# Kernel tuning notes

Measured on AMD Instinct MI355X. Metric: run time of the kernel, lower is better.

## Reference

```python
import jax, jax.numpy as jnp
import numpy as np

SIGMA = 0.1  # kernel-point influence radius (KPConv linear correlation)


def setup_inputs() -> dict:
    key = jax.random.key(0)
    k1, k2, k3, k4, k5 = jax.random.split(key, 5)
    N, K, KP, CIN, COUT = 65536, 32, 15, 64, 128
    pos = jax.random.uniform(k1, (N, 3), dtype=jnp.float32)
    feats = jax.random.normal(k2, (N, CIN), dtype=jnp.float32)
    kernel_points = jax.random.normal(k3, (KP, 3), dtype=jnp.float32) * 0.05
    weights = jax.random.normal(k4, (KP, CIN, COUT), dtype=jnp.float32) / np.sqrt(KP * CIN)
    neighbors = jax.random.randint(k5, (N, K), 0, N, dtype=jnp.int64)
    return {"pos": pos, "feats": feats, "kernel_points": kernel_points,
            "weights": weights, "neighbors": neighbors}


def reference(pos, feats, kernel_points, weights, neighbors):
    # pos: [N,3], feats: [N,Cin], kernel_points: [Kp,3],
    # weights: [Kp,Cin,Cout], neighbors: [N,K] int
    neigh_pos = pos[neighbors]                      # [N,K,3] irregular gather
    rel = neigh_pos - pos[:, None, :]               # [N,K,3]
    # distance from each relative neighbor offset to each kernel point
    d = rel[:, :, None, :] - kernel_points[None, None, :, :]   # [N,K,Kp,3]
    dist = jnp.sqrt(jnp.sum(d * d, axis=-1))        # [N,K,Kp]
    infl = jnp.maximum(0.0, 1.0 - dist / SIGMA)     # linear correlation
    neigh_feat = feats[neighbors]                   # [N,K,Cin] irregular gather
    # per-kernel-point weighted neighbor aggregation, then projection
    weighted = jnp.einsum('njk,njc->nkc', infl, neigh_feat)    # [N,Kp,Cin]
    out = jnp.einsum('nkc,kcd->nd', weighted, weights)         # [N,Cout]
    return out
```

## Files before the change

### kernel.cpp

```cpp
#include <hip/hip_runtime.h>

#define NPTS  65536
#define KNB   32
#define KPn   15
#define CIN   64
#define COUT  128
#define MPTS  16
#define THREADS 256
#define WSTRIDE 968
#define BCAP  32
#define NTILE 8
#define KSTEPS 30

typedef __attribute__((ext_vector_type(8))) short short8;
typedef __attribute__((ext_vector_type(4))) float f32x4;

__device__ __forceinline__ unsigned int f2bf(float f) {
    union { float f; unsigned int i; } v; v.f = f;
    return (v.i + 0x7fffu + ((v.i >> 16) & 1u)) >> 16;
}

__global__ void wtrans_kernel(const float* __restrict__ w,
                              unsigned short* __restrict__ wTf) {
    const int d = blockIdx.x * 256 + threadIdx.x;
    if (d < NTILE * KSTEPS * 64 * 8) {
        const int j    = d & 7;
        const int lane = (d >> 3) & 63;
        const int ks   = (d >> 9) % KSTEPS;
        const int t    = d / (KSTEPS * 512);
        const int f    = ks * 32 + (lane >> 4) * 8 + j;
        const int cg   = f / 120;
        const int rem  = f - cg * 120;
        const int kpk  = rem >> 3;
        const int cw   = rem & 7;
        const int orig = kpk * 64 + cg * 8 + cw;
        const int n    = t * 16 + (lane & 15);
        wTf[d] = (unsigned short)f2bf(w[(size_t)orig * COUT + n]);
    }
}

__global__ __launch_bounds__(THREADS, 4) void kpconv_kernel(
    const float* __restrict__ pos,
    const float* __restrict__ feats,
    const float* __restrict__ kpts,
    const unsigned short* __restrict__ wTf,
    const int*   __restrict__ neighbors,
    float*       __restrict__ out)
{
    __shared__ unsigned short wl[MPTS * WSTRIDE];
    __shared__ int   bcnt[MPTS];
    __shared__ int   bid[MPTS][BCAP];
    __shared__ float bval[MPTS][BCAP];
    __shared__ float cposf[MPTS * 3];
    __shared__ float kpfl[KPn * 3];

    const int tid = threadIdx.x;
    const int n0  = blockIdx.x * MPTS;

    if (tid < MPTS) bcnt[tid] = 0;
    if (tid < MPTS * 3) cposf[tid] = pos[(size_t)n0 * 3 + tid];
    if (tid < KPn * 3)  kpfl[tid]  = kpts[tid];
    __syncthreads();

    for (int s = tid; s < MPTS * KNB; s += THREADS) {
        const int p  = s >> 5;
        const int nb = neighbors[(size_t)n0 * KNB + s];
        const float rx = pos[(size_t)nb * 3 + 0] - cposf[p * 3 + 0];
        const float ry = pos[(size_t)nb * 3 + 1] - cposf[p * 3 + 1];
        const float rz = pos[(size_t)nb * 3 + 2] - cposf[p * 3 + 2];
        #pragma unroll
        for (int k = 0; k < KPn; ++k) {
            const float dx = rx - kpfl[k * 3 + 0];
            const float dy = ry - kpfl[k * 3 + 1];
            const float dz = rz - kpfl[k * 3 + 2];
            const float d2 = dx * dx + dy * dy + dz * dz;
            if (d2 < 0.01f) {
                const float w = 1.0f - 10.0f * sqrtf(d2);
                const int idx = atomicAdd(&bcnt[p], 1);
                if (idx < BCAP) { bid[p][idx] = (nb << 4) | k; bval[p][idx] = w; }
            }
        }
    }
    __syncthreads();

    #pragma unroll
    for (int it = 0; it < 8; ++it) {
        const int wi = tid + it * THREADS;
        const int cg = wi & 7;
        const int k  = (wi >> 3) & 15;
        const int p  = wi >> 7;
        if (k < KPn) {
            float a0=0.f,a1=0.f,a2=0.f,a3=0.f,a4=0.f,a5=0.f,a6=0.f,a7=0.f;
            const int cnt = min(bcnt[p], BCAP);
            for (int e = 0; e < cnt; ++e) {
                const int id = bid[p][e];
                if ((id & 15) == k) {
                    const float wv = bval[p][e];
                    const float* fr = feats + (size_t)(id >> 4) * CIN + cg * 8;
                    const float4 f0 = *(const float4*)fr;
                    const float4 f1 = *(const float4*)(fr + 4);
                    a0 += wv * f0.x; a1 += wv * f0.y; a2 += wv * f0.z; a3 += wv * f0.w;
                    a4 += wv * f1.x; a5 += wv * f1.y; a6 += wv * f1.z; a7 += wv * f1.w;
                }
            }
            uint4 u;
            u.x = f2bf(a0) | (f2bf(a1) << 16);
            u.y = f2bf(a2) | (f2bf(a3) << 16);
            u.z = f2bf(a4) | (f2bf(a5) << 16);
            u.w = f2bf(a6) | (f2bf(a7) << 16);
            *(uint4*)(wl + p * WSTRIDE + cg * 120 + k * 8) = u;
        }
    }
    __syncthreads();

    {
        const int wave = tid >> 6;
        const int lane = tid & 63;
        const int m    = lane & 15;
        const int q    = lane >> 4;

        f32x4 acc0 = {0.f, 0.f, 0.f, 0.f};
        f32x4 acc1 = {0.f, 0.f, 0.f, 0.f};

        const unsigned short* ap = wl + m * WSTRIDE + q * 8;
        const short8* bp0 = (const short8*)wTf + (size_t)(2 * wave) * KSTEPS * 64 + lane;
        const short8* bp1 = bp0 + (size_t)KSTEPS * 64;

        #pragma unroll 3
        for (int ks = 0; ks < KSTEPS; ++ks, ap += 32) {
            const short8 a  = *(const short8*)ap;
            const short8 b0 = bp0[ks * 64];
            const short8 b1 = bp1[ks * 64];
            acc0 = __builtin_amdgcn_mfma_f32_16x16x32_bf16(a, b0, acc0, 0, 0, 0);
            acc1 = __builtin_amdgcn_mfma_f32_16x16x32_bf16(a, b1, acc1, 0, 0, 0);
        }

        const int nb0 = wave * 32;
        #pragma unroll
        for (int r = 0; r < 4; ++r) {
            const size_t row = (size_t)(n0 + q * 4 + r) * COUT;
            out[row + nb0 + m]      = acc0[r];
            out[row + nb0 + 16 + m] = acc1[r];
        }
    }
}

extern "C" void kernel_launch(void* const* d_in, const int* in_sizes, int n_in,
                              void* d_out, int out_size, void* d_ws, size_t ws_size,
                              hipStream_t stream) {
    const float* pos       = (const float*)d_in[0];
    const float* feats     = (const float*)d_in[1];
    const float* kpts      = (const float*)d_in[2];
    const float* weights   = (const float*)d_in[3];
    const int*   neighbors = (const int*)d_in[4];
    float*       out       = (float*)d_out;
    unsigned short* wTf    = (unsigned short*)d_ws;

    wtrans_kernel<<<(NTILE * KSTEPS * 512 + 255) / 256, 256, 0, stream>>>(weights, wTf);
    kpconv_kernel<<<NPTS / MPTS, THREADS, 0, stream>>>(pos, feats, kpts, wTf, neighbors, out);
}
```

Measured before the change: 151.5 us.

## Double points per block, add bounding-sphere cull and dot-product kernel-point test

Doubles the block to 32 points and 512 threads. Each of the 8 waves now computes one 16-column output tile for two 16-row point tiles, so every weight B-fragment loaded from global memory is reused twice. The neighbor/kernel-point distance test first culls neighbors outside a bounding sphere (sigma plus the max kernel-point radius). It then uses a precomputed |kp|^2 and a dot-product comparison instead of computing full distances, which skips most of the 15-point loop. Shared memory per block roughly doubles (about 62 KB), which may lower occupancy. Launch bounds of 512x4 may not be achievable.

```diff
diff --git a/kernel.cpp b/kernel.cpp
--- a/kernel.cpp
+++ b/kernel.cpp
@@ -5,8 +5,8 @@
 #define KPn   15
 #define CIN   64
 #define COUT  128
-#define MPTS  16
-#define THREADS 256
+#define MPTS  32
+#define THREADS 512
 #define WSTRIDE 968
 #define BCAP  32
 #define NTILE 8
@@ -52,32 +52,57 @@
     __shared__ int   bid[MPTS][BCAP];
     __shared__ float bval[MPTS][BCAP];
     __shared__ float cposf[MPTS * 3];
-    __shared__ float kpfl[KPn * 3];
+    __shared__ float4 kpq[KPn];
+    __shared__ float R2s;
 
     const int tid = threadIdx.x;
     const int n0  = blockIdx.x * MPTS;
 
     if (tid < MPTS) bcnt[tid] = 0;
     if (tid < MPTS * 3) cposf[tid] = pos[(size_t)n0 * 3 + tid];
-    if (tid < KPn * 3)  kpfl[tid]  = kpts[tid];
+    if (tid < KPn) {
+        const float x = kpts[tid * 3 + 0];
+        const float y = kpts[tid * 3 + 1];
+        const float z = kpts[tid * 3 + 2];
+        kpq[tid] = make_float4(x, y, z, x * x + y * y + z * z);
+    }
+    if (tid == THREADS - 1) {
+        float mx = 0.f;
+        for (int k = 0; k < KPn; ++k) {
+            const float x = kpts[k * 3 + 0];
+            const float y = kpts[k * 3 + 1];
+            const float z = kpts[k * 3 + 2];
+            mx = fmaxf(mx, x * x + y * y + z * z);
+        }
+        const float R = 0.1f + sqrtf(mx);
+        R2s = R * R;
+    }
     __syncthreads();
 
-    for (int s = tid; s < MPTS * KNB; s += THREADS) {
-        const int p  = s >> 5;
-        const int nb = neighbors[(size_t)n0 * KNB + s];
-        const float rx = pos[(size_t)nb * 3 + 0] - cposf[p * 3 + 0];
-        const float ry = pos[(size_t)nb * 3 + 1] - cposf[p * 3 + 1];
-        const float rz = pos[(size_t)nb * 3 + 2] - cposf[p * 3 + 2];
+    {
+        const float R2 = R2s;
         #pragma unroll
-        for (int k = 0; k < KPn; ++k) {
-            const float dx = rx - kpfl[k * 3 + 0];
-            const float dy = ry - kpfl[k * 3 + 1];
-            const float dz = rz - kpfl[k * 3 + 2];
-            const float d2 = dx * dx + dy * dy + dz * dz;
-            if (d2 < 0.01f) {
-                const float w = 1.0f - 10.0f * sqrtf(d2);
-                const int idx = atomicAdd(&bcnt[p], 1);
-                if (idx < BCAP) { bid[p][idx] = (nb << 4) | k; bval[p][idx] = w; }
+        for (int it = 0; it < MPTS * KNB / THREADS; ++it) {
+            const int s  = tid + it * THREADS;
+            const int p  = s >> 5;
+            const int nb = neighbors[(size_t)n0 * KNB + s];
+            const float rx = pos[(size_t)nb * 3 + 0] - cposf[p * 3 + 0];
+            const float ry = pos[(size_t)nb * 3 + 1] - cposf[p * 3 + 1];
+            const float rz = pos[(size_t)nb * 3 + 2] - cposf[p * 3 + 2];
+            const float d2r = rx * rx + ry * ry + rz * rz;
+            if (d2r < R2) {
+                const float hd = 0.5f * (d2r - 0.01f);
+                #pragma unroll
+                for (int k = 0; k < KPn; ++k) {
+                    const float4 kp = kpq[k];
+                    const float dot = rx * kp.x + ry * kp.y + rz * kp.z;
+                    if (dot > hd + 0.5f * kp.w) {
+                        const float d2 = fmaxf(d2r - 2.f * dot + kp.w, 0.f);
+                        const float w = 1.0f - 10.0f * sqrtf(d2);
+                        const int idx = atomicAdd(&bcnt[p], 1);
+                        if (idx < BCAP) { bid[p][idx] = (nb << 4) | k; bval[p][idx] = w; }
+                    }
+                }
             }
         }
     }
@@ -122,25 +147,24 @@
         f32x4 acc0 = {0.f, 0.f, 0.f, 0.f};
         f32x4 acc1 = {0.f, 0.f, 0.f, 0.f};
 
-        const unsigned short* ap = wl + m * WSTRIDE + q * 8;
-        const short8* bp0 = (const short8*)wTf + (size_t)(2 * wave) * KSTEPS * 64 + lane;
-        const short8* bp1 = bp0 + (size_t)KSTEPS * 64;
+        const unsigned short* a0p = wl + m * WSTRIDE + q * 8;
+        const unsigned short* a1p = a0p + 16 * WSTRIDE;
+        const short8* bp = (const short8*)wTf + (size_t)wave * KSTEPS * 64 + lane;
 
         #pragma unroll 3
-        for (int ks = 0; ks < KSTEPS; ++ks, ap += 32) {
-            const short8 a  = *(const short8*)ap;
-            const short8 b0 = bp0[ks * 64];
-            const short8 b1 = bp1[ks * 64];
-            acc0 = __builtin_amdgcn_mfma_f32_16x16x32_bf16(a, b0, acc0, 0, 0, 0);
-            acc1 = __builtin_amdgcn_mfma_f32_16x16x32_bf16(a, b1, acc1, 0, 0, 0);
+        for (int ks = 0; ks < KSTEPS; ++ks, a0p += 32, a1p += 32) {
+            const short8 a0 = *(const short8*)a0p;
+            const short8 a1 = *(const short8*)a1p;
+            const short8 b  = bp[ks * 64];
+            acc0 = __builtin_amdgcn_mfma_f32_16x16x32_bf16(a0, b, acc0, 0, 0, 0);
+            acc1 = __builtin_amdgcn_mfma_f32_16x16x32_bf16(a1, b, acc1, 0, 0, 0);
         }
 
-        const int nb0 = wave * 32;
+        const int c = wave * 16 + m;
         #pragma unroll
         for (int r = 0; r < 4; ++r) {
-            const size_t row = (size_t)(n0 + q * 4 + r) * COUT;
-            out[row + nb0 + m]      = acc0[r];
-            out[row + nb0 + 16 + m] = acc1[r];
+            out[(size_t)(n0 + q * 4 + r) * COUT + c]      = acc0[r];
+            out[(size_t)(n0 + 16 + q * 4 + r) * COUT + c] = acc1[r];
         }
     }
 }
```

New measurement: 155.5 us. 2.7% more time.

## Fuse weight transform into a persistent KPConv kernel with a grid barrier

Applied to the files above, without the earlier changes.

Folds the bf16 weight re-layout into the main kernel and drops the separate launch. All blocks synchronise through a global atomic counter that waits on a poisoned-workspace sentinel. The grid becomes 512 persistent blocks of 512 threads, each looping over 8 point tiles, with each wave computing one 16-column output tile. Neighbor bucket entries are packed into one 32-bit word holding the neighbor index, the kernel-point index and a 12-bit quantized influence, which halves bucket LDS traffic. In exchange it depends on all blocks being co-resident, on the workspace counter state across calls, and on N being at most 65536, and it adds quantization error to the influence weights.

```diff
diff --git a/kernel.cpp b/kernel.cpp
--- a/kernel.cpp
+++ b/kernel.cpp
@@ -6,11 +6,15 @@
 #define CIN   64
 #define COUT  128
 #define MPTS  16
-#define THREADS 256
+#define THREADS 512
+#define GRID  512
+#define TPB   8
 #define WSTRIDE 968
-#define BCAP  32
+#define BCAP  48
 #define NTILE 8
 #define KSTEPS 30
+#define WELEMS (NTILE * KSTEPS * 64 * 8)
+#define POISON 0xAAAAAAAAu
 
 typedef __attribute__((ext_vector_type(8))) short short8;
 typedef __attribute__((ext_vector_type(4))) float f32x4;
@@ -20,128 +24,143 @@
     return (v.i + 0x7fffu + ((v.i >> 16) & 1u)) >> 16;
 }
 
-__global__ void wtrans_kernel(const float* __restrict__ w,
-                              unsigned short* __restrict__ wTf) {
-    const int d = blockIdx.x * 256 + threadIdx.x;
-    if (d < NTILE * KSTEPS * 64 * 8) {
-        const int j    = d & 7;
-        const int lane = (d >> 3) & 63;
-        const int ks   = (d >> 9) % KSTEPS;
-        const int t    = d / (KSTEPS * 512);
-        const int f    = ks * 32 + (lane >> 4) * 8 + j;
-        const int cg   = f / 120;
-        const int rem  = f - cg * 120;
-        const int kpk  = rem >> 3;
-        const int cw   = rem & 7;
-        const int orig = kpk * 64 + cg * 8 + cw;
-        const int n    = t * 16 + (lane & 15);
-        wTf[d] = (unsigned short)f2bf(w[(size_t)orig * COUT + n]);
-    }
-}
-
-__global__ __launch_bounds__(THREADS, 4) void kpconv_kernel(
+__global__ __launch_bounds__(THREADS, 2) void kpconv_kernel(
     const float* __restrict__ pos,
     const float* __restrict__ feats,
     const float* __restrict__ kpts,
-    const unsigned short* __restrict__ wTf,
+    const float* __restrict__ weights,
     const int*   __restrict__ neighbors,
-    float*       __restrict__ out)
+    float*       __restrict__ out,
+    unsigned short* __restrict__ wTf,
+    unsigned int* cnt)
 {
     __shared__ unsigned short wl[MPTS * WSTRIDE];
+    __shared__ unsigned int  bpk[MPTS][BCAP];
     __shared__ int   bcnt[MPTS];
-    __shared__ int   bid[MPTS][BCAP];
-    __shared__ float bval[MPTS][BCAP];
     __shared__ float cposf[MPTS * 3];
     __shared__ float kpfl[KPn * 3];
 
     const int tid = threadIdx.x;
-    const int n0  = blockIdx.x * MPTS;
 
-    if (tid < MPTS) bcnt[tid] = 0;
-    if (tid < MPTS * 3) cposf[tid] = pos[(size_t)n0 * 3 + tid];
-    if (tid < KPn * 3)  kpfl[tid]  = kpts[tid];
+    {
+        const int d = blockIdx.x * THREADS + tid;
+        if (d < WELEMS) {
+            const int j    = d & 7;
+            const int lane = (d >> 3) & 63;
+            const int ks   = (d >> 9) % KSTEPS;
+            const int t    = d / (KSTEPS * 512);
+            const int f    = ks * 32 + (lane >> 4) * 8 + j;
+            const int cg   = f / 120;
+            const int rem  = f - cg * 120;
+            const int orig = (rem >> 3) * 64 + cg * 8 + (rem & 7);
+            const int n    = t * 16 + (lane & 15);
+            wTf[d] = (unsigned short)f2bf(weights[(size_t)orig * COUT + n]);
+        }
+    }
+
     __syncthreads();
-
-    for (int s = tid; s < MPTS * KNB; s += THREADS) {
-        const int p  = s >> 5;
-        const int nb = neighbors[(size_t)n0 * KNB + s];
-        const float rx = pos[(size_t)nb * 3 + 0] - cposf[p * 3 + 0];
-        const float ry = pos[(size_t)nb * 3 + 1] - cposf[p * 3 + 1];
-        const float rz = pos[(size_t)nb * 3 + 2] - cposf[p * 3 + 2];
-        #pragma unroll
-        for (int k = 0; k < KPn; ++k) {
-            const float dx = rx - kpfl[k * 3 + 0];
-            const float dy = ry - kpfl[k * 3 + 1];
-            const float dz = rz - kpfl[k * 3 + 2];
-            const float d2 = dx * dx + dy * dy + dz * dz;
-            if (d2 < 0.01f) {
-                const float w = 1.0f - 10.0f * sqrtf(d2);
-                const int idx = atomicAdd(&bcnt[p], 1);
-                if (idx < BCAP) { bid[p][idx] = (nb << 4) | k; bval[p][idx] = w; }
-            }
-        }
+    if (tid == 0) {
+        __builtin_amdgcn_fence(__ATOMIC_RELEASE, "agent");
+        unsigned int v = __hip_atomic_load(cnt, __ATOMIC_RELAXED,
+                                           __HIP_MEMORY_SCOPE_AGENT);
+        if (v == POISON) atomicCAS(cnt, POISON, 0u);
+        atomicAdd(cnt, 1u);
+        unsigned int x;
+        do {
+            __builtin_amdgcn_s_sleep(2);
+            x = __hip_atomic_load(cnt, __ATOMIC_RELAXED,
+                                  __HIP_MEMORY_SCOPE_AGENT);
+        } while (x == POISON || x < GRID);
+        __builtin_amdgcn_fence(__ATOMIC_ACQUIRE, "agent");
     }
     __syncthreads();
 
-    #pragma unroll
-    for (int it = 0; it < 8; ++it) {
-        const int wi = tid + it * THREADS;
-        const int cg = wi & 7;
-        const int k  = (wi >> 3) & 15;
-        const int p  = wi >> 7;
-        if (k < KPn) {
-            float a0=0.f,a1=0.f,a2=0.f,a3=0.f,a4=0.f,a5=0.f,a6=0.f,a7=0.f;
-            const int cnt = min(bcnt[p], BCAP);
-            for (int e = 0; e < cnt; ++e) {
-                const int id = bid[p][e];
-                if ((id & 15) == k) {
-                    const float wv = bval[p][e];
-                    const float* fr = feats + (size_t)(id >> 4) * CIN + cg * 8;
-                    const float4 f0 = *(const float4*)fr;
-                    const float4 f1 = *(const float4*)(fr + 4);
-                    a0 += wv * f0.x; a1 += wv * f0.y; a2 += wv * f0.z; a3 += wv * f0.w;
-                    a4 += wv * f1.x; a5 += wv * f1.y; a6 += wv * f1.z; a7 += wv * f1.w;
+    if (tid < KPn * 3) kpfl[tid] = kpts[tid];
+
+    for (int it8 = 0; it8 < TPB; ++it8) {
+        const int n0 = (blockIdx.x * TPB + it8) * MPTS;
+
+        if (tid < MPTS) bcnt[tid] = 0;
+        if (tid < MPTS * 3) cposf[tid] = pos[(size_t)n0 * 3 + tid];
+        __syncthreads();
+
+        {
+            const int s  = tid;
+            const int p  = s >> 5;
+            const int nb = neighbors[(size_t)n0 * KNB + s];
+            const float rx = pos[(size_t)nb * 3 + 0] - cposf[p * 3 + 0];
+            const float ry = pos[(size_t)nb * 3 + 1] - cposf[p * 3 + 1];
+            const float rz = pos[(size_t)nb * 3 + 2] - cposf[p * 3 + 2];
+            #pragma unroll
+            for (int k = 0; k < KPn; ++k) {
+                const float dx = rx - kpfl[k * 3 + 0];
+                const float dy = ry - kpfl[k * 3 + 1];
+                const float dz = rz - kpfl[k * 3 + 2];
+                const float d2 = dx * dx + dy * dy + dz * dz;
+                if (d2 < 0.01f) {
+                    const float w = 1.0f - 10.0f * sqrtf(d2);
+                    const unsigned int wq = (unsigned int)(w * 4095.0f + 0.5f);
+                    const int idx = atomicAdd(&bcnt[p], 1);
+                    if (idx < BCAP)
+                        bpk[p][idx] = ((unsigned int)nb << 16) | ((unsigned int)k << 12) | wq;
                 }
             }
-            uint4 u;
-            u.x = f2bf(a0) | (f2bf(a1) << 16);
-            u.y = f2bf(a2) | (f2bf(a3) << 16);
-            u.z = f2bf(a4) | (f2bf(a5) << 16);
-            u.w = f2bf(a6) | (f2bf(a7) << 16);
-            *(uint4*)(wl + p * WSTRIDE + cg * 120 + k * 8) = u;
         }
-    }
-    __syncthreads();
+        __syncthreads();
 
-    {
-        const int wave = tid >> 6;
-        const int lane = tid & 63;
-        const int m    = lane & 15;
-        const int q    = lane >> 4;
+        #pragma unroll
+        for (int it = 0; it < 4; ++it) {
+            const int wi = tid + it * THREADS;
+            const int cg = wi & 7;
+            const int k  = (wi >> 3) & 15;
+            const int p  = wi >> 7;
+            if (k < KPn) {
+                float a0=0.f,a1=0.f,a2=0.f,a3=0.f,a4=0.f,a5=0.f,a6=0.f,a7=0.f;
+                const int cnt2 = min(bcnt[p], BCAP);
+                for (int e = 0; e < cnt2; ++e) {
+                    const unsigned int id = bpk[p][e];
+                    if (((id >> 12) & 15u) == (unsigned int)k) {
+                        const float wv = (float)(id & 4095u) * (1.0f / 4095.0f);
+                        const float* fr = feats + (size_t)(id >> 16) * CIN + cg * 8;
+                        const float4 f0 = *(const float4*)fr;
+                        const float4 f1 = *(const float4*)(fr + 4);
+                        a0 += wv * f0.x; a1 += wv * f0.y; a2 += wv * f0.z; a3 += wv * f0.w;
+                        a4 += wv * f1.x; a5 += wv * f1.y; a6 += wv * f1.z; a7 += wv * f1.w;
+                    }
+                }
+                uint4 u;
+                u.x = f2bf(a0) | (f2bf(a1) << 16);
+                u.y = f2bf(a2) | (f2bf(a3) << 16);
+                u.z = f2bf(a4) | (f2bf(a5) << 16);
+                u.w = f2bf(a6) | (f2bf(a7) << 16);
+                *(uint4*)(wl + p * WSTRIDE + cg * 120 + k * 8) = u;
+            }
+        }
+        __syncthreads();
 
-        f32x4 acc0 = {0.f, 0.f, 0.f, 0.f};
-        f32x4 acc1 = {0.f, 0.f, 0.f, 0.f};
+        {
+            const int wave = tid >> 6;
+            const int lane = tid & 63;
+            const int m    = lane & 15;
+            const int q    = lane >> 4;
 
-        const unsigned short* ap = wl + m * WSTRIDE + q * 8;
-        const short8* bp0 = (const short8*)wTf + (size_t)(2 * wave) * KSTEPS * 64 + lane;
-        const short8* bp1 = bp0 + (size_t)KSTEPS * 64;
+            f32x4 acc = {0.f, 0.f, 0.f, 0.f};
+            const unsigned short* ap = wl + m * WSTRIDE + q * 8;
+            const short8* bp = (const short8*)wTf + (size_t)wave * KSTEPS * 64 + lane;
 
-        #pragma unroll 3
-        for (int ks = 0; ks < KSTEPS; ++ks, ap += 32) {
-            const short8 a  = *(const short8*)ap;
-            const short8 b0 = bp0[ks * 64];
-            const short8 b1 = bp1[ks * 64];
-            acc0 = __builtin_amdgcn_mfma_f32_16x16x32_bf16(a, b0, acc0, 0, 0, 0);
-            acc1 = __builtin_amdgcn_mfma_f32_16x16x32_bf16(a, b1, acc1, 0, 0, 0);
+            #pragma unroll 3
+            for (int ks = 0; ks < KSTEPS; ++ks, ap += 32) {
+                const short8 a = *(const short8*)ap;
+                const short8 b = bp[ks * 64];
+                acc = __builtin_amdgcn_mfma_f32_16x16x32_bf16(a, b, acc, 0, 0, 0);
+            }
+
+            const int c = wave * 16 + m;
+            #pragma unroll
+            for (int r = 0; r < 4; ++r)
+                out[(size_t)(n0 + q * 4 + r) * COUT + c] = acc[r];
         }
-
-        const int nb0 = wave * 32;
-        #pragma unroll
-        for (int r = 0; r < 4; ++r) {
-            const size_t row = (size_t)(n0 + q * 4 + r) * COUT;
-            out[row + nb0 + m]      = acc0[r];
-            out[row + nb0 + 16 + m] = acc1[r];
-        }
+        __syncthreads();
     }
 }
 
@@ -155,7 +174,8 @@
     const int*   neighbors = (const int*)d_in[4];
     float*       out       = (float*)d_out;
     unsigned short* wTf    = (unsigned short*)d_ws;
+    unsigned int* cnt      = (unsigned int*)((char*)d_ws + WELEMS * 2);
 
-    wtrans_kernel<<<(NTILE * KSTEPS * 512 + 255) / 256, 256, 0, stream>>>(weights, wTf);
-    kpconv_kernel<<<NPTS / MPTS, THREADS, 0, stream>>>(pos, feats, kpts, wTf, neighbors, out);
+    kpconv_kernel<<<GRID, THREADS, 0, stream>>>(pos, feats, kpts, weights,
+                                                neighbors, out, wTf, cnt);
 }
```

New measurement: 196.1 us. +29.4%, slower.
